# Kernel optimization log

Measured on AMD Instinct MI355X. Metric: run time of the kernel, lower is better.

## Reference

```python
import math
import jax, jax.numpy as jnp
import numpy as np

B, T, QDIM, ADIM = 256, 2048, 1024, 128
DC, DK = 8, 21          # dynamic channels / kernel
SC, SK = 8, 21          # static channels / kernel
PL, ALPHA, BETA = 11, 0.1, 0.9


def _betabinom_pmf_flipped(n, a, b, length):
    lg = np.vectorize(math.lgamma)
    k = np.arange(length, dtype=np.float64)
    logp = (lg(n + 1.0) - lg(k + 1.0) - lg(n - k + 1.0)
            + lg(k + a) + lg(n - k + b) - lg(n + a + b)
            - (lg(a) + lg(b) - lg(a + b)))
    return np.exp(logp)[::-1].copy()  # .flip(0) as in the torch buffer


def setup_inputs() -> dict:
    key = jax.random.key(0)
    ks = jax.random.split(key, 10)

    def lin(k, shape, fan_in):
        return (jax.random.normal(k, shape, jnp.float32) / np.sqrt(fan_in)).astype(jnp.float32)

    query = jax.random.normal(ks[0], (B, QDIM), jnp.float32)
    # previous-step alignment: a valid probability distribution over T
    alignment_pre = jax.nn.softmax(2.0 * jax.random.normal(ks[1], (B, T), jnp.float32), axis=1)

    P = jnp.asarray(_betabinom_pmf_flipped(PL - 1, ALPHA, BETA, PL), jnp.float32)
    W_w = lin(ks[2], (ADIM, QDIM), QDIM)
    W_b = jnp.zeros((ADIM,), jnp.float32)
    V_w = lin(ks[3], (DC * DK, ADIM), ADIM)
    F_w = lin(ks[4], (SC, 1, SK), SK)        # Conv1d(1, SC, SK) weight
    U_w = lin(ks[5], (ADIM, SC), SC)
    T_w = lin(ks[6], (ADIM, DC), DC)
    T_b = jnp.zeros((ADIM,), jnp.float32)
    v_w = lin(ks[7], (1, ADIM), ADIM)
    return {"query": query, "alignment_pre": alignment_pre, "P": P,
            "W_w": W_w, "W_b": W_b, "V_w": V_w, "F_w": F_w,
            "U_w": U_w, "T_w": T_w, "T_b": T_b, "v_w": v_w}


def reference(query, alignment_pre, P, W_w, W_b, V_w, F_w, U_w, T_w, T_b, v_w):
    b, t = alignment_pre.shape
    pad = (DK - 1) // 2  # == PL - 1 == 10, shared by all three convs
    x_pad = jnp.pad(alignment_pre, ((0, 0), (pad, pad)))
    # sliding windows (cross-correlation layout): windows[b, t, k] = x_pad[b, t + k]
    windows = jnp.stack([x_pad[:, k:k + t] for k in range(DK)], axis=-1)  # (B, T, DK)

    # prior: causal conv with left pad PL-1 == windows taps 0..PL-1
    p = jnp.log(jnp.clip(jnp.einsum('btk,k->bt', windows[..., :PL], P), 1e-6))

    # per-sample dynamic kernels
    G = jnp.tanh(query @ W_w.T + W_b) @ V_w.T          # (B, DC*DK)
    G = G.reshape(b, DC, DK)
    g = jnp.einsum('btk,bck->btc', windows, G)          # grouped conv, groups=B -> (B, T, DC)

    # static conv over previous alignment
    f = jnp.einsum('btk,ck->btc', windows, F_w[:, 0, :])  # (B, T, SC)

    e = jnp.squeeze(jnp.tanh(f @ U_w.T + g @ T_w.T + T_b) @ v_w.T, -1) + p  # (B, T)
    return jax.nn.softmax(e, axis=1)
```

## Files before the change

kernel.cpp:

```cpp
#include <hip/hip_runtime.h>
#include <hip/hip_bf16.h>

#define Bsz 256
#define Tn 2048
#define QD 1024
#define AD 128
#define DCn 8
#define DKn 21
#define PLn 11
#define GN (DCn * DKn)
#define XS2 24

typedef _Float16 f16x8 __attribute__((ext_vector_type(8)));
typedef float f32x4 __attribute__((ext_vector_type(4)));

__global__ __launch_bounds__(512) void g_kernel(
    const float* __restrict__ query, const float* __restrict__ W_w,
    const float* __restrict__ W_b, const float* __restrict__ V_w,
    float* __restrict__ G_ws)
{
    __shared__ float h_lds[AD];
    const int b    = blockIdx.x;
    const int tid  = threadIdx.x;
    const int w    = tid >> 6;
    const int lane = tid & 63;

    const float4* q4 = (const float4*)(query + b * QD);
    float4 q0 = q4[lane];
    float4 q1 = q4[64 + lane];
    float4 q2 = q4[128 + lane];
    float4 q3 = q4[192 + lane];

    #pragma unroll 2
    for (int i = 0; i < 16; ++i) {
        int a = w * 16 + i;
        const float4* w4 = (const float4*)(W_w + a * QD);
        float4 x0 = w4[lane];
        float4 x1 = w4[64 + lane];
        float4 x2 = w4[128 + lane];
        float4 x3 = w4[192 + lane];
        float accA = 0.f, accB = 0.f;
        accA = fmaf(q0.x, x0.x, fmaf(q0.y, x0.y, fmaf(q0.z, x0.z, fmaf(q0.w, x0.w, accA))));
        accB = fmaf(q1.x, x1.x, fmaf(q1.y, x1.y, fmaf(q1.z, x1.z, fmaf(q1.w, x1.w, accB))));
        accA = fmaf(q2.x, x2.x, fmaf(q2.y, x2.y, fmaf(q2.z, x2.z, fmaf(q2.w, x2.w, accA))));
        accB = fmaf(q3.x, x3.x, fmaf(q3.y, x3.y, fmaf(q3.z, x3.z, fmaf(q3.w, x3.w, accB))));
        float acc = accA + accB;
        #pragma unroll
        for (int off = 32; off; off >>= 1) acc += __shfl_xor(acc, off);
        if (lane == 0) h_lds[a] = tanhf(acc + W_b[a]);
    }
    __syncthreads();

    for (int r = w; r < GN; r += 8) {
        float acc = fmaf(h_lds[lane], V_w[r * AD + lane],
                         h_lds[64 + lane] * V_w[r * AD + 64 + lane]);
        #pragma unroll
        for (int off = 32; off; off >>= 1) acc += __shfl_xor(acc, off);
        if (lane == 0) G_ws[b * GN + r] = acc;
    }
}

__global__ __launch_bounds__(1024, 4) void e_kernel(
    const float* __restrict__ align, const float* __restrict__ P,
    const float* __restrict__ F_w, const float* __restrict__ U_w,
    const float* __restrict__ T_w, const float* __restrict__ T_b,
    const float* __restrict__ v_w, const float* __restrict__ G_ws,
    float* __restrict__ out)
{
    __shared__ float    al32[Tn + 20];
    __shared__ _Float16 al16[Tn + 44];
    __shared__ float    pcb[Tn];
    __shared__ float    sden[Tn];
    __shared__ _Float16 Xw[16 * 16 * XS2];
    __shared__ float    red[16];
    __shared__ float    bc;

    const int b    = blockIdx.x;
    const int tid  = threadIdx.x;
    const int lane = tid & 63;
    const int wid  = tid >> 6;
    const int l15  = lane & 15;
    const int quad = lane >> 4;

    for (int i = tid; i < Tn + 44; i += 1024) {
        int s = i - 10;
        float v = (s >= 0 && s < Tn) ? align[b * Tn + s] : 0.f;
        if (i < Tn + 20) al32[i] = v;
        al16[i] = (_Float16)v;
    }

    f16x8 Bc = {};
    #pragma unroll
    for (int j = 0; j < 8; ++j) {
        int k = quad * 8 + j;
        float wv = 0.f;
        if (k < DKn) wv = (l15 < 8) ? F_w[l15 * DKn + k]
                                    : G_ws[b * GN + (l15 - 8) * DKn + k];
        Bc[j] = (_Float16)wv;
    }

    f16x8 Bf[8];
    float vv[8], tb[8];
    #pragma unroll
    for (int n = 0; n < 8; ++n) {
        int a = n * 16 + l15;
        f16x8 bf = {};
        const float* src = (quad == 0) ? (U_w + a * 8) : (T_w + a * 8);
        if (quad < 2) {
            float4 lo = ((const float4*)src)[0];
            float4 hi = ((const float4*)src)[1];
            bf[0] = (_Float16)(2.f * lo.x); bf[1] = (_Float16)(2.f * lo.y);
            bf[2] = (_Float16)(2.f * lo.z); bf[3] = (_Float16)(2.f * lo.w);
            bf[4] = (_Float16)(2.f * hi.x); bf[5] = (_Float16)(2.f * hi.y);
            bf[6] = (_Float16)(2.f * hi.z); bf[7] = (_Float16)(2.f * hi.w);
        }
        Bf[n] = bf;
        vv[n] = v_w[a];
        tb[n] = 2.f * T_b[a];
    }
    __syncthreads();

    #pragma unroll
    for (int tt = 0; tt < 2; ++tt) {
        int t = tid + tt * 1024;
        float pr = 0.f;
        #pragma unroll
        for (int k = 0; k < PLn; ++k) pr = fmaf(al32[t + k], P[k], pr);
        pcb[t] = fmaxf(pr, 1e-6f);
    }
    __syncthreads();

    const int t0w = wid * 128;
    _Float16* Xp = &Xw[wid * 16 * XS2];
    float wsum = 0.f;

    for (int m = 0; m < 8; ++m) {
        const int t0 = t0w + m * 16;

        f16x8 Ac;
        #pragma unroll
        for (int j = 0; j < 8; ++j) Ac[j] = al16[t0 + l15 + quad * 8 + j];

        f32x4 z = {};
        f32x4 Xd = __builtin_amdgcn_mfma_f32_16x16x32_f16(Ac, Bc, z, 0, 0, 0);

        #pragma unroll
        for (int r = 0; r < 4; ++r)
            Xp[(quad * 4 + r) * XS2 + l15] = (_Float16)Xd[r];

        asm volatile("s_waitcnt lgkmcnt(0)" ::: "memory");

        f16x8 A2 = {};
        if (quad < 2) A2 = *(const f16x8*)&Xp[l15 * XS2 + quad * 8];

        float es0 = 0.f, es1 = 0.f, es2 = 0.f, es3 = 0.f;
        #pragma unroll
        for (int n = 0; n < 8; ++n) {
            f32x4 z2 = {};
            f32x4 d = __builtin_amdgcn_mfma_f32_16x16x32_f16(A2, Bf[n], z2, 0, 0, 0);
            float q0 = __expf(d[0] + tb[n]);
            float q1 = __expf(d[1] + tb[n]);
            float q2 = __expf(d[2] + tb[n]);
            float q3 = __expf(d[3] + tb[n]);
            float r0 = __builtin_amdgcn_rcpf(q0 + 1.f);
            float r1 = __builtin_amdgcn_rcpf(q1 + 1.f);
            float r2 = __builtin_amdgcn_rcpf(q2 + 1.f);
            float r3 = __builtin_amdgcn_rcpf(q3 + 1.f);
            es0 = fmaf(vv[n], fmaf(-2.f, r0, 1.f), es0);
            es1 = fmaf(vv[n], fmaf(-2.f, r1, 1.f), es1);
            es2 = fmaf(vv[n], fmaf(-2.f, r2, 1.f), es2);
            es3 = fmaf(vv[n], fmaf(-2.f, r3, 1.f), es3);
        }
        #pragma unroll
        for (int off = 1; off <= 8; off <<= 1) {
            es0 += __shfl_xor(es0, off);
            es1 += __shfl_xor(es1, off);
            es2 += __shfl_xor(es2, off);
            es3 += __shfl_xor(es3, off);
        }
        if (l15 < 4) {
            float ev = (l15 == 0) ? es0 : (l15 == 1) ? es1 : (l15 == 2) ? es2 : es3;
            int t = t0 + quad * 4 + l15;
            float sv = pcb[t] * __expf(ev);
            sden[t] = sv;
            wsum += sv;
        }
    }

    __syncthreads();
    #pragma unroll
    for (int off = 32; off; off >>= 1) wsum += __shfl_xor(wsum, off);
    if (lane == 0) red[wid] = wsum;
    __syncthreads();
    if (wid == 0) {
        float ss = (lane < 16) ? red[lane] : 0.f;
        #pragma unroll
        for (int off = 8; off; off >>= 1) ss += __shfl_xor(ss, off);
        if (lane == 0) bc = ss;
    }
    __syncthreads();
    const float inv = 1.f / bc;
    out[b * Tn + tid]        = sden[tid] * inv;
    out[b * Tn + tid + 1024] = sden[tid + 1024] * inv;
}

extern "C" void kernel_launch(void* const* d_in, const int* in_sizes, int n_in,
                              void* d_out, int out_size, void* d_ws, size_t ws_size,
                              hipStream_t stream) {
    const float* query = (const float*)d_in[0];
    const float* align = (const float*)d_in[1];
    const float* P     = (const float*)d_in[2];
    const float* W_w   = (const float*)d_in[3];
    const float* W_b   = (const float*)d_in[4];
    const float* V_w   = (const float*)d_in[5];
    const float* F_w   = (const float*)d_in[6];
    const float* U_w   = (const float*)d_in[7];
    const float* T_w   = (const float*)d_in[8];
    const float* T_b   = (const float*)d_in[9];
    const float* v_w   = (const float*)d_in[10];
    float* out  = (float*)d_out;
    float* G_ws = (float*)d_ws;

    g_kernel<<<Bsz, 512, 0, stream>>>(query, W_w, W_b, V_w, G_ws);
    e_kernel<<<Bsz, 1024, 0, stream>>>(align, P, F_w, U_w, T_w, T_b, v_w, G_ws, out);
}
```

Measured before the change: 123.4 us.

## Interleave two time tiles per iteration and fold tanh constants into exp2 weights

The e_kernel main loop now handles two 16-step tiles per iteration. It issues paired MFMAs and paired exp/rcp chains so that independent work can hide MFMA and transcendental latency, with a double-sized LDS scratch buffer. The 2*log2(e) factor is folded into the U/T weights and bias so the native exp2 can be used. The tanh rewrite is simplified by precomputing -2*v and adding the sum of v once after the reduction. The explicit lgkmcnt wait becomes a compiler memory barrier, and the changes raise register and LDS pressure.

```diff
diff --git a/kernel.cpp b/kernel.cpp
--- a/kernel.cpp
+++ b/kernel.cpp
@@ -13,6 +13,8 @@
 
 typedef _Float16 f16x8 __attribute__((ext_vector_type(8)));
 typedef float f32x4 __attribute__((ext_vector_type(4)));
+
+#define TWO_LOG2E 2.8853900817779268f
 
 __global__ __launch_bounds__(512) void g_kernel(
     const float* __restrict__ query, const float* __restrict__ W_w,
@@ -71,7 +73,7 @@
     __shared__ _Float16 al16[Tn + 44];
     __shared__ float    pcb[Tn];
     __shared__ float    sden[Tn];
-    __shared__ _Float16 Xw[16 * 16 * XS2];
+    __shared__ _Float16 Xw[16 * 2 * 16 * XS2];
     __shared__ float    red[16];
     __shared__ float    bc;
 
@@ -100,7 +102,8 @@
     }
 
     f16x8 Bf[8];
-    float vv[8], tb[8];
+    float vn2[8], tb2[8];
+    float vsum = 0.f;
     #pragma unroll
     for (int n = 0; n < 8; ++n) {
         int a = n * 16 + l15;
@@ -109,15 +112,19 @@
         if (quad < 2) {
             float4 lo = ((const float4*)src)[0];
             float4 hi = ((const float4*)src)[1];
-            bf[0] = (_Float16)(2.f * lo.x); bf[1] = (_Float16)(2.f * lo.y);
-            bf[2] = (_Float16)(2.f * lo.z); bf[3] = (_Float16)(2.f * lo.w);
-            bf[4] = (_Float16)(2.f * hi.x); bf[5] = (_Float16)(2.f * hi.y);
-            bf[6] = (_Float16)(2.f * hi.z); bf[7] = (_Float16)(2.f * hi.w);
+            bf[0] = (_Float16)(TWO_LOG2E * lo.x); bf[1] = (_Float16)(TWO_LOG2E * lo.y);
+            bf[2] = (_Float16)(TWO_LOG2E * lo.z); bf[3] = (_Float16)(TWO_LOG2E * lo.w);
+            bf[4] = (_Float16)(TWO_LOG2E * hi.x); bf[5] = (_Float16)(TWO_LOG2E * hi.y);
+            bf[6] = (_Float16)(TWO_LOG2E * hi.z); bf[7] = (_Float16)(TWO_LOG2E * hi.w);
         }
         Bf[n] = bf;
-        vv[n] = v_w[a];
-        tb[n] = 2.f * T_b[a];
-    }
+        float va = v_w[a];
+        vn2[n] = -2.f * va;
+        vsum  += va;
+        tb2[n] = TWO_LOG2E * T_b[a];
+    }
+    #pragma unroll
+    for (int off = 1; off <= 8; off <<= 1) vsum += __shfl_xor(vsum, off);
     __syncthreads();
 
     #pragma unroll
@@ -131,59 +138,75 @@
     __syncthreads();
 
     const int t0w = wid * 128;
-    _Float16* Xp = &Xw[wid * 16 * XS2];
+    _Float16* Xp0 = &Xw[wid * 2 * 16 * XS2];
+    _Float16* Xp1 = Xp0 + 16 * XS2;
     float wsum = 0.f;
 
-    for (int m = 0; m < 8; ++m) {
-        const int t0 = t0w + m * 16;
-
-        f16x8 Ac;
-        #pragma unroll
-        for (int j = 0; j < 8; ++j) Ac[j] = al16[t0 + l15 + quad * 8 + j];
-
+    #pragma unroll 1
+    for (int m = 0; m < 8; m += 2) {
+        const int ta = t0w + m * 16;
+        const int tb_ = ta + 16;
+
+        f16x8 Ac0, Ac1;
+        #pragma unroll
+        for (int j = 0; j < 8; ++j) {
+            Ac0[j] = al16[ta  + l15 + quad * 8 + j];
+            Ac1[j] = al16[tb_ + l15 + quad * 8 + j];
+        }
         f32x4 z = {};
-        f32x4 Xd = __builtin_amdgcn_mfma_f32_16x16x32_f16(Ac, Bc, z, 0, 0, 0);
-
-        #pragma unroll
-        for (int r = 0; r < 4; ++r)
-            Xp[(quad * 4 + r) * XS2 + l15] = (_Float16)Xd[r];
-
-        asm volatile("s_waitcnt lgkmcnt(0)" ::: "memory");
-
-        f16x8 A2 = {};
-        if (quad < 2) A2 = *(const f16x8*)&Xp[l15 * XS2 + quad * 8];
-
-        float es0 = 0.f, es1 = 0.f, es2 = 0.f, es3 = 0.f;
+        f32x4 X0 = __builtin_amdgcn_mfma_f32_16x16x32_f16(Ac0, Bc, z, 0, 0, 0);
+        f32x4 X1 = __builtin_amdgcn_mfma_f32_16x16x32_f16(Ac1, Bc, z, 0, 0, 0);
+
+        #pragma unroll
+        for (int r = 0; r < 4; ++r) {
+            Xp0[(quad * 4 + r) * XS2 + l15] = (_Float16)X0[r];
+            Xp1[(quad * 4 + r) * XS2 + l15] = (_Float16)X1[r];
+        }
+        __asm__ __volatile__("" ::: "memory");
+
+        f16x8 A20 = {}, A21 = {};
+        if (quad < 2) {
+            A20 = *(const f16x8*)&Xp0[l15 * XS2 + quad * 8];
+            A21 = *(const f16x8*)&Xp1[l15 * XS2 + quad * 8];
+        }
+
+        float esA[4] = {0.f, 0.f, 0.f, 0.f};
+        float esB[4] = {0.f, 0.f, 0.f, 0.f};
         #pragma unroll
         for (int n = 0; n < 8; ++n) {
             f32x4 z2 = {};
-            f32x4 d = __builtin_amdgcn_mfma_f32_16x16x32_f16(A2, Bf[n], z2, 0, 0, 0);
-            float q0 = __expf(d[0] + tb[n]);
-            float q1 = __expf(d[1] + tb[n]);
-            float q2 = __expf(d[2] + tb[n]);
-            float q3 = __expf(d[3] + tb[n]);
-            float r0 = __builtin_amdgcn_rcpf(q0 + 1.f);
-            float r1 = __builtin_amdgcn_rcpf(q1 + 1.f);
-            float r2 = __builtin_amdgcn_rcpf(q2 + 1.f);
-            float r3 = __builtin_amdgcn_rcpf(q3 + 1.f);
-            es0 = fmaf(vv[n], fmaf(-2.f, r0, 1.f), es0);
-            es1 = fmaf(vv[n], fmaf(-2.f, r1, 1.f), es1);
-            es2 = fmaf(vv[n], fmaf(-2.f, r2, 1.f), es2);
-            es3 = fmaf(vv[n], fmaf(-2.f, r3, 1.f), es3);
+            f32x4 d0 = __builtin_amdgcn_mfma_f32_16x16x32_f16(A20, Bf[n], z2, 0, 0, 0);
+            f32x4 d1 = __builtin_amdgcn_mfma_f32_16x16x32_f16(A21, Bf[n], z2, 0, 0, 0);
+            #pragma unroll
+            for (int r = 0; r < 4; ++r) {
+                float qa = __builtin_amdgcn_exp2f(d0[r] + tb2[n]);
+                float qb = __builtin_amdgcn_exp2f(d1[r] + tb2[n]);
+                float ra = __builtin_amdgcn_rcpf(qa + 1.f);
+                float rb = __builtin_amdgcn_rcpf(qb + 1.f);
+                esA[r] = fmaf(vn2[n], ra, esA[r]);
+                esB[r] = fmaf(vn2[n], rb, esB[r]);
+            }
         }
         #pragma unroll
         for (int off = 1; off <= 8; off <<= 1) {
-            es0 += __shfl_xor(es0, off);
-            es1 += __shfl_xor(es1, off);
-            es2 += __shfl_xor(es2, off);
-            es3 += __shfl_xor(es3, off);
+            #pragma unroll
+            for (int r = 0; r < 4; ++r) {
+                esA[r] += __shfl_xor(esA[r], off);
+                esB[r] += __shfl_xor(esB[r], off);
+            }
         }
         if (l15 < 4) {
-            float ev = (l15 == 0) ? es0 : (l15 == 1) ? es1 : (l15 == 2) ? es2 : es3;
-            int t = t0 + quad * 4 + l15;
-            float sv = pcb[t] * __expf(ev);
-            sden[t] = sv;
-            wsum += sv;
+            float evA = ((l15 == 0) ? esA[0] : (l15 == 1) ? esA[1]
+                       : (l15 == 2) ? esA[2] : esA[3]) + vsum;
+            float evB = ((l15 == 0) ? esB[0] : (l15 == 1) ? esB[1]
+                       : (l15 == 2) ? esB[2] : esB[3]) + vsum;
+            int tA = ta  + quad * 4 + l15;
+            int tB = tb_ + quad * 4 + l15;
+            float svA = pcb[tA] * __expf(evA);
+            float svB = pcb[tB] * __expf(evB);
+            sden[tA] = svA;
+            sden[tB] = svB;
+            wsum += svA + svB;
         }
     }
 
```

Result: faster. 120.1 us (-2.7%).
